# Optimization experiments

Measured on AMD Instinct MI355X. Metric: run time of the kernel, lower is better.

## Reference

```python
import jax, jax.numpy as jnp
import numpy as np

N_NODES = 50000
N_EDGES = 800000
D = 512
N_LAYERS = 3
LN_EPS = 1e-5


def _layer_norm(h, gamma, beta):
    mu = jnp.mean(h, axis=-1, keepdims=True)
    var = jnp.mean(jnp.square(h - mu), axis=-1, keepdims=True)
    return (h - mu) * jax.lax.rsqrt(var + LN_EPS) * gamma + beta


def setup_inputs() -> dict:
    key = jax.random.key(0)
    ks = jax.random.split(key, 5)
    x = jax.random.normal(ks[0], (N_NODES, D), dtype=jnp.float32)
    edge_index = jax.random.randint(ks[1], (2, N_EDGES), 0, N_NODES, dtype=jnp.int64)
    edge_weight = jax.random.uniform(ks[2], (N_EDGES,), dtype=jnp.float32)
    # GCNConv lin weights (xavier-ish scale), zero biases; LayerNorm affine params
    Ws = jax.random.normal(ks[3], (N_LAYERS, D, D), dtype=jnp.float32) * (1.0 / np.sqrt(D))
    bs = jnp.zeros((N_LAYERS, D), dtype=jnp.float32)
    gammas = jnp.ones((N_LAYERS, D), dtype=jnp.float32)
    betas = jnp.zeros((N_LAYERS, D), dtype=jnp.float32)
    return {"x": x, "edge_index": edge_index, "edge_weight": edge_weight,
            "Ws": Ws, "bs": bs, "gammas": gammas, "betas": betas}


def reference(x, edge_index, edge_weight, Ws, bs, gammas, betas):
    n = x.shape[0]
    row, col = edge_index[0], edge_index[1]  # source -> target (PyG convention)
    # add self loops with weight 1 (GCNConv add_self_loops=True)
    sl = jnp.arange(n, dtype=edge_index.dtype)
    row2 = jnp.concatenate([row, sl])
    col2 = jnp.concatenate([col, sl])
    ew = jnp.concatenate([edge_weight, jnp.ones((n,), dtype=edge_weight.dtype)])
    # symmetric normalization: D^{-1/2} A D^{-1/2}
    deg = jax.ops.segment_sum(ew, col2, num_segments=n)
    dinv = jnp.where(deg > 0, 1.0 / jnp.sqrt(jnp.where(deg > 0, deg, 1.0)), 0.0)
    norm = dinv[row2] * ew * dinv[col2]  # [E+N]

    for i in range(N_LAYERS):
        identity = x
        h = x @ Ws[i].T                       # [N, D] linear transform
        msg = norm[:, None] * h[row2]         # gather + scale per edge
        agg = jax.ops.segment_sum(msg, col2, num_segments=n) + bs[i]
        h = _layer_norm(agg, gammas[i], betas[i])
        if i < N_LAYERS - 1:
            h = jax.nn.relu(h)                # dropout=0 -> identity
        x = h + identity                      # residual (dims equal -> Identity proj)
    return x
```

## Files before the change

kernel.cpp:

```cpp
#include <hip/hip_runtime.h>
#include <hip/hip_bf16.h>
#include <stdint.h>

#define D 512
#define LN_EPS 1e-5f

typedef __attribute__((ext_vector_type(8))) short bf16x8;
typedef __attribute__((ext_vector_type(4))) float f32x4;

__device__ __forceinline__ unsigned short f32_to_bf16_bits(float x) {
    unsigned int u = __float_as_uint(x);
    u += 0x7fffu + ((u >> 16) & 1u);
    return (unsigned short)(u >> 16);
}
__device__ __forceinline__ float bf16lo(unsigned int u) { return __uint_as_float(u << 16); }
__device__ __forceinline__ float bf16hi(unsigned int u) { return __uint_as_float(u & 0xffff0000u); }

typedef const __attribute__((address_space(1))) unsigned int GU;
typedef __attribute__((address_space(3))) unsigned int LU;
__device__ __forceinline__ void gload_lds16(const void* g, void* l) {
    __builtin_amdgcn_global_load_lds((GU*)g, (LU*)l, 16, 0, 0);
}

__global__ void k_prep(const float4* __restrict__ x0, ushort4* __restrict__ xb4,
                       const float4* __restrict__ Ws4, ushort4* __restrict__ wb4,
                       float* __restrict__ deg, int* __restrict__ cnt,
                       long nx4, long nxin4, long nw4, int N) {
    long id = (long)blockIdx.x * blockDim.x + threadIdx.x;
    if (id < nx4) {
        float4 v;
        if (id < nxin4) v = x0[id];
        else { v.x = 0.f; v.y = 0.f; v.z = 0.f; v.w = 0.f; }
        ushort4 o;
        o.x = f32_to_bf16_bits(v.x);
        o.y = f32_to_bf16_bits(v.y);
        o.z = f32_to_bf16_bits(v.z);
        o.w = f32_to_bf16_bits(v.w);
        xb4[id] = o;
    } else if (id < nx4 + nw4) {
        long i = id - nx4;
        float4 v = Ws4[i];
        ushort4 o;
        o.x = f32_to_bf16_bits(v.x);
        o.y = f32_to_bf16_bits(v.y);
        o.z = f32_to_bf16_bits(v.z);
        o.w = f32_to_bf16_bits(v.w);
        wb4[i] = o;
    } else {
        long i = id - nx4 - nw4;
        if (i < N) { deg[i] = 1.0f; cnt[i] = 1; }
    }
}

__global__ void k_deg_cnt(const int* __restrict__ col, const float* __restrict__ ew,
                          float* deg, int* cnt, int E) {
    int e = blockIdx.x * blockDim.x + threadIdx.x;
    if (e < E) {
        int c = col[e];
        atomicAdd(&deg[c], ew[e]);
        atomicAdd(&cnt[c], 1);
    }
}

__global__ __launch_bounds__(1024) void k_scan(const int* __restrict__ cnt,
                                               float* __restrict__ deg,
                                               int* __restrict__ rptr,
                                               int* __restrict__ cur, int n) {
    for (int i = threadIdx.x; i < n; i += 1024) deg[i] = rsqrtf(deg[i]);

    const int tid = threadIdx.x, lane = tid & 63, wv = tid >> 6;
    const int chunk = (n + 15) >> 4;
    const int wbeg = wv * chunk;
    const int wend = min(wbeg + chunk, n);

    int tot = 0;
    for (int i = wbeg + lane; i < wend; i += 64) tot += cnt[i];
#pragma unroll
    for (int off = 32; off > 0; off >>= 1) tot += __shfl_xor(tot, off);
    __shared__ int woff[17];
    if (lane == 0) woff[wv] = tot;
    __syncthreads();
    if (tid == 0) {
        int r = 0;
        for (int w = 0; w < 16; ++w) { int t = woff[w]; woff[w] = r; r += t; }
        woff[16] = r;
    }
    __syncthreads();

    int run = woff[wv];
    for (int base = wbeg; base < wend; base += 64) {
        int i = base + lane;
        int v = (i < wend) ? cnt[i] : 0;
        int inc = v;
#pragma unroll
        for (int off = 1; off < 64; off <<= 1) {
            int u = __shfl_up(inc, off);
            if (lane >= off) inc += u;
        }
        if (i < wend) {
            int excl = run + inc - v;
            rptr[i] = excl;
            cur[i] = excl;
        }
        run += __shfl(inc, 63);
    }
    if (tid == 0) rptr[n] = woff[16];
}

__global__ void k_fill(const int* __restrict__ row, const int* __restrict__ col,
                       const float* __restrict__ ew, const float* __restrict__ dinv,
                       int* cur, uint2* __restrict__ srcval, int N, int E) {
    int i = blockIdx.x * blockDim.x + threadIdx.x;
    if (i < N) {
        int slot = atomicAdd(&cur[i], 1);
        float d = dinv[i];
        uint2 sv; sv.x = (unsigned)i; sv.y = __float_as_uint(d * d);
        srcval[slot] = sv;
    } else if (i < N + E) {
        int e = i - N;
        int r = row[e], c = col[e];
        int slot = atomicAdd(&cur[c], 1);
        uint2 sv; sv.x = (unsigned)r;
        sv.y = __float_as_uint(dinv[r] * ew[e] * dinv[c]);
        srcval[slot] = sv;
    }
}

__global__ __launch_bounds__(512) void k_gemm(
    const short* __restrict__ A,
    const short* __restrict__ W,
    short* __restrict__ H,
    int Mpad) {
    __shared__ short As[2][128 * 32];
    __shared__ short Bs[2][256 * 32];
    const int tid = threadIdx.x;
    const int wave = tid >> 6, lane = tid & 63;
    const int wm = (wave >> 2) * 64, wn = (wave & 3) * 64;
    const int tm = blockIdx.x * 128, tn = blockIdx.y * 256;
    f32x4 acc[4][4] = {};
    const int fr = lane & 15, fc = lane >> 4;

    const int r0 = tid >> 2, cb0 = (tid & 3) * 8;
    const short* Ab = A + (size_t)(tm + r0) * 512 + cb0;
    const short* Wb = W + (size_t)(tn + r0) * 512 + cb0;

    gload_lds16(Ab,                     &As[0][tid * 8]);
    gload_lds16(Wb,                     &Bs[0][tid * 8]);
    gload_lds16(Wb + (size_t)128 * 512, &Bs[0][(tid + 512) * 8]);
    __syncthreads();

    int cur = 0;
    for (int k0 = 0; k0 < 512; k0 += 32) {
        const int kn = k0 + 32;
        if (kn < 512) {
            gload_lds16(Ab + kn,                     &As[cur ^ 1][tid * 8]);
            gload_lds16(Wb + kn,                     &Bs[cur ^ 1][tid * 8]);
            gload_lds16(Wb + (size_t)128 * 512 + kn, &Bs[cur ^ 1][(tid + 512) * 8]);
        }
        bf16x8 af[4], bfr[4];
#pragma unroll
        for (int m = 0; m < 4; ++m)
            af[m] = *(const bf16x8*)&As[cur][(wm + m * 16 + fr) * 32 + fc * 8];
#pragma unroll
        for (int n = 0; n < 4; ++n)
            bfr[n] = *(const bf16x8*)&Bs[cur][(wn + n * 16 + fr) * 32 + fc * 8];
#pragma unroll
        for (int m = 0; m < 4; ++m) {
#pragma unroll
            for (int n = 0; n < 4; ++n)
                acc[m][n] = __builtin_amdgcn_mfma_f32_16x16x32_bf16(af[m], bfr[n], acc[m][n], 0, 0, 0);
        }
        __syncthreads();
        cur ^= 1;
    }
    const int cbase = tn + wn + (lane & 15);
    const int rbase = tm + wm + fc * 4;
#pragma unroll
    for (int m = 0; m < 4; ++m) {
#pragma unroll
        for (int n = 0; n < 4; ++n) {
#pragma unroll
            for (int j = 0; j < 4; ++j) {
                int r = rbase + m * 16 + j;
                int c = cbase + n * 16;
                H[(size_t)r * 512 + c] = (short)f32_to_bf16_bits(acc[m][n][j]);
            }
        }
    }
}

__global__ __launch_bounds__(256) void k_agg_ln(
    const uint4* __restrict__ H4,
    const int* __restrict__ rptr,
    const uint2* __restrict__ srcval,
    const float4* __restrict__ bias,
    const float4* __restrict__ gamma,
    const float4* __restrict__ beta,
    uint4* __restrict__ xb,
    float4* __restrict__ out_f32,
    int N, int last) {
    const int wv = threadIdx.x >> 6, lane = threadIdx.x & 63;
    const int t = blockIdx.x * 4 + wv;
    if (t >= N) return;
    const int beg = rptr[t], end = rptr[t + 1];

    float a[8], b[8];
#pragma unroll
    for (int i = 0; i < 8; ++i) { a[i] = 0.f; b[i] = 0.f; }

    for (int base = beg; base < end; base += 64) {
        int m = end - base;
        if (m > 64) m = 64;
        int idx = base + lane;
        if (idx > end - 1) idx = end - 1;
        uint2 svl = srcval[idx];
        int e = 0;
        for (; e + 2 <= m; e += 2) {
            unsigned s0 = __shfl(svl.x, e);
            unsigned s1 = __shfl(svl.x, e + 1);
            float w0 = __uint_as_float(__shfl(svl.y, e));
            float w1 = __uint_as_float(__shfl(svl.y, e + 1));
            uint4 u0 = H4[(size_t)s0 * 64 + lane];
            uint4 u1 = H4[(size_t)s1 * 64 + lane];
            a[0] = fmaf(w0, bf16lo(u0.x), a[0]);
            a[1] = fmaf(w0, bf16hi(u0.x), a[1]);
            a[2] = fmaf(w0, bf16lo(u0.y), a[2]);
            a[3] = fmaf(w0, bf16hi(u0.y), a[3]);
            a[4] = fmaf(w0, bf16lo(u0.z), a[4]);
            a[5] = fmaf(w0, bf16hi(u0.z), a[5]);
            a[6] = fmaf(w0, bf16lo(u0.w), a[6]);
            a[7] = fmaf(w0, bf16hi(u0.w), a[7]);
            b[0] = fmaf(w1, bf16lo(u1.x), b[0]);
            b[1] = fmaf(w1, bf16hi(u1.x), b[1]);
            b[2] = fmaf(w1, bf16lo(u1.y), b[2]);
            b[3] = fmaf(w1, bf16hi(u1.y), b[3]);
            b[4] = fmaf(w1, bf16lo(u1.z), b[4]);
            b[5] = fmaf(w1, bf16hi(u1.z), b[5]);
            b[6] = fmaf(w1, bf16lo(u1.w), b[6]);
            b[7] = fmaf(w1, bf16hi(u1.w), b[7]);
        }
        if (e < m) {
            unsigned s0 = __shfl(svl.x, e);
            float w0 = __uint_as_float(__shfl(svl.y, e));
            uint4 u0 = H4[(size_t)s0 * 64 + lane];
            a[0] = fmaf(w0, bf16lo(u0.x), a[0]);
            a[1] = fmaf(w0, bf16hi(u0.x), a[1]);
            a[2] = fmaf(w0, bf16lo(u0.y), a[2]);
            a[3] = fmaf(w0, bf16hi(u0.y), a[3]);
            a[4] = fmaf(w0, bf16lo(u0.z), a[4]);
            a[5] = fmaf(w0, bf16hi(u0.z), a[5]);
            a[6] = fmaf(w0, bf16lo(u0.w), a[6]);
            a[7] = fmaf(w0, bf16hi(u0.w), a[7]);
        }
    }
#pragma unroll
    for (int i = 0; i < 8; ++i) a[i] += b[i];

    float4 bv0 = bias[lane * 2], bv1 = bias[lane * 2 + 1];
    a[0] += bv0.x; a[1] += bv0.y; a[2] += bv0.z; a[3] += bv0.w;
    a[4] += bv1.x; a[5] += bv1.y; a[6] += bv1.z; a[7] += bv1.w;

    float s1 = 0.f, s2 = 0.f;
#pragma unroll
    for (int i = 0; i < 8; ++i) { s1 += a[i]; s2 += a[i] * a[i]; }
#pragma unroll
    for (int off = 32; off > 0; off >>= 1) {
        s1 += __shfl_xor(s1, off);
        s2 += __shfl_xor(s2, off);
    }
    const float mean = s1 * (1.0f / 512.0f);
    const float var = s2 * (1.0f / 512.0f) - mean * mean;
    const float rstd = rsqrtf(var + LN_EPS);

    float4 gv0 = gamma[lane * 2], gv1 = gamma[lane * 2 + 1];
    float4 bt0 = beta[lane * 2], bt1 = beta[lane * 2 + 1];
    float o[8];
    o[0] = (a[0] - mean) * rstd * gv0.x + bt0.x;
    o[1] = (a[1] - mean) * rstd * gv0.y + bt0.y;
    o[2] = (a[2] - mean) * rstd * gv0.z + bt0.z;
    o[3] = (a[3] - mean) * rstd * gv0.w + bt0.w;
    o[4] = (a[4] - mean) * rstd * gv1.x + bt1.x;
    o[5] = (a[5] - mean) * rstd * gv1.y + bt1.y;
    o[6] = (a[6] - mean) * rstd * gv1.z + bt1.z;
    o[7] = (a[7] - mean) * rstd * gv1.w + bt1.w;
    if (!last) {
#pragma unroll
        for (int i = 0; i < 8; ++i) o[i] = fmaxf(o[i], 0.f);
    }
    uint4 idu = xb[(size_t)t * 64 + lane];
    o[0] += bf16lo(idu.x); o[1] += bf16hi(idu.x);
    o[2] += bf16lo(idu.y); o[3] += bf16hi(idu.y);
    o[4] += bf16lo(idu.z); o[5] += bf16hi(idu.z);
    o[6] += bf16lo(idu.w); o[7] += bf16hi(idu.w);

    if (last) {
        float4 f0, f1;
        f0.x = o[0]; f0.y = o[1]; f0.z = o[2]; f0.w = o[3];
        f1.x = o[4]; f1.y = o[5]; f1.z = o[6]; f1.w = o[7];
        out_f32[(size_t)t * 128 + lane * 2] = f0;
        out_f32[(size_t)t * 128 + lane * 2 + 1] = f1;
    } else {
        uint4 pk;
        pk.x = ((unsigned)f32_to_bf16_bits(o[1]) << 16) | f32_to_bf16_bits(o[0]);
        pk.y = ((unsigned)f32_to_bf16_bits(o[3]) << 16) | f32_to_bf16_bits(o[2]);
        pk.z = ((unsigned)f32_to_bf16_bits(o[5]) << 16) | f32_to_bf16_bits(o[4]);
        pk.w = ((unsigned)f32_to_bf16_bits(o[7]) << 16) | f32_to_bf16_bits(o[6]);
        xb[(size_t)t * 64 + lane] = pk;
    }
}

extern "C" void kernel_launch(void* const* d_in, const int* in_sizes, int n_in,
                              void* d_out, int out_size, void* d_ws, size_t ws_size,
                              hipStream_t stream) {
    const float* x0     = (const float*)d_in[0];
    const int*   ei     = (const int*)d_in[1];
    const float* ew     = (const float*)d_in[2];
    const float* Ws     = (const float*)d_in[3];
    const float* bs     = (const float*)d_in[4];
    const float* gammas = (const float*)d_in[5];
    const float* betas  = (const float*)d_in[6];

    const int N = in_sizes[0] / D;
    const int E = in_sizes[1] / 2;
    const int L = in_sizes[3] / (D * D);
    const int Mpad = (N + 127) & ~127;

    char* p = (char*)d_ws;
    auto carve = [&](size_t bytes) {
        char* q = p;
        p += (bytes + 255) & ~(size_t)255;
        return (void*)q;
    };
    short* xb     = (short*)carve((size_t)Mpad * D * 2);
    short* hb     = (short*)carve((size_t)Mpad * D * 2);
    short* wb     = (short*)carve((size_t)L * D * D * 2);
    float* dinv   = (float*)carve((size_t)N * 4);
    int*   cnt    = (int*)carve((size_t)N * 4);
    int*   rptr   = (int*)carve((size_t)(N + 1) * 4);
    int*   cur    = (int*)carve((size_t)N * 4);
    uint2* srcval = (uint2*)carve((size_t)(E + N) * 8);
    (void)ws_size; (void)n_in; (void)out_size;

    const int* rowI = ei;
    const int* colI = ei + E;

    {
        long nx4 = (long)Mpad * D / 4, nxin4 = (long)N * D / 4;
        long nw4 = (long)L * D * D / 4;
        long tot = nx4 + nw4 + N;
        k_prep<<<(int)((tot + 255) / 256), 256, 0, stream>>>(
            (const float4*)x0, (ushort4*)xb, (const float4*)Ws, (ushort4*)wb,
            dinv, cnt, nx4, nxin4, nw4, N);
    }
    k_deg_cnt<<<(E + 255) / 256, 256, 0, stream>>>(colI, ew, dinv, cnt, E);
    k_scan<<<1, 1024, 0, stream>>>(cnt, dinv, rptr, cur, N);
    k_fill<<<(N + E + 255) / 256, 256, 0, stream>>>(rowI, colI, ew, dinv, cur, srcval, N, E);

    for (int l = 0; l < L; ++l) {
        dim3 g(Mpad / 128, D / 256);
        k_gemm<<<g, 512, 0, stream>>>(xb, wb + (size_t)l * D * D, hb, Mpad);
        int last = (l == L - 1);
        k_agg_ln<<<(N + 3) / 4, 256, 0, stream>>>(
            (const uint4*)hb, rptr, srcval,
            (const float4*)(bs + (size_t)l * D),
            (const float4*)(gammas + (size_t)l * D),
            (const float4*)(betas + (size_t)l * D),
            (uint4*)xb, (float4*)d_out, N, last);
    }
}
```

Measured before the change: 700.2 us.

## Aggregate before the linear transform and fuse LayerNorm into the GEMM epilogue

Uses linearity to compute the sparse aggregation on the bf16 node features first, then multiplies by W. Each GEMM block now covers all 512 output columns, so bias, LayerNorm (row stats reduced via LDS), ReLU and the residual run in the GEMM epilogue. This replaces the separate pass over the GEMM output. In exchange, each GEMM block holds twice the accumulators and LDS and there are half as many blocks, which risks load imbalance and lower occupancy. The epilogue also reads and writes xb as scattered 2-byte elements.

Result: slower. 893.3 us (+27.6%).

```diff
diff --git a/kernel.cpp b/kernel.cpp
--- a/kernel.cpp
+++ b/kernel.cpp
@@ -15,6 +15,7 @@
 }
 __device__ __forceinline__ float bf16lo(unsigned int u) { return __uint_as_float(u << 16); }
 __device__ __forceinline__ float bf16hi(unsigned int u) { return __uint_as_float(u & 0xffff0000u); }
+__device__ __forceinline__ float bf16s(short s) { return __uint_as_float(((unsigned int)(unsigned short)s) << 16); }
 
 typedef const __attribute__((address_space(1))) unsigned int GU;
 typedef __attribute__((address_space(3))) unsigned int LU;
@@ -126,79 +127,12 @@
     }
 }
 
-__global__ __launch_bounds__(512) void k_gemm(
-    const short* __restrict__ A,
-    const short* __restrict__ W,
-    short* __restrict__ H,
-    int Mpad) {
-    __shared__ short As[2][128 * 32];
-    __shared__ short Bs[2][256 * 32];
-    const int tid = threadIdx.x;
-    const int wave = tid >> 6, lane = tid & 63;
-    const int wm = (wave >> 2) * 64, wn = (wave & 3) * 64;
-    const int tm = blockIdx.x * 128, tn = blockIdx.y * 256;
-    f32x4 acc[4][4] = {};
-    const int fr = lane & 15, fc = lane >> 4;
-
-    const int r0 = tid >> 2, cb0 = (tid & 3) * 8;
-    const short* Ab = A + (size_t)(tm + r0) * 512 + cb0;
-    const short* Wb = W + (size_t)(tn + r0) * 512 + cb0;
-
-    gload_lds16(Ab,                     &As[0][tid * 8]);
-    gload_lds16(Wb,                     &Bs[0][tid * 8]);
-    gload_lds16(Wb + (size_t)128 * 512, &Bs[0][(tid + 512) * 8]);
-    __syncthreads();
-
-    int cur = 0;
-    for (int k0 = 0; k0 < 512; k0 += 32) {
-        const int kn = k0 + 32;
-        if (kn < 512) {
-            gload_lds16(Ab + kn,                     &As[cur ^ 1][tid * 8]);
-            gload_lds16(Wb + kn,                     &Bs[cur ^ 1][tid * 8]);
-            gload_lds16(Wb + (size_t)128 * 512 + kn, &Bs[cur ^ 1][(tid + 512) * 8]);
-        }
-        bf16x8 af[4], bfr[4];
-#pragma unroll
-        for (int m = 0; m < 4; ++m)
-            af[m] = *(const bf16x8*)&As[cur][(wm + m * 16 + fr) * 32 + fc * 8];
-#pragma unroll
-        for (int n = 0; n < 4; ++n)
-            bfr[n] = *(const bf16x8*)&Bs[cur][(wn + n * 16 + fr) * 32 + fc * 8];
-#pragma unroll
-        for (int m = 0; m < 4; ++m) {
-#pragma unroll
-            for (int n = 0; n < 4; ++n)
-                acc[m][n] = __builtin_amdgcn_mfma_f32_16x16x32_bf16(af[m], bfr[n], acc[m][n], 0, 0, 0);
-        }
-        __syncthreads();
-        cur ^= 1;
-    }
-    const int cbase = tn + wn + (lane & 15);
-    const int rbase = tm + wm + fc * 4;
-#pragma unroll
-    for (int m = 0; m < 4; ++m) {
-#pragma unroll
-        for (int n = 0; n < 4; ++n) {
-#pragma unroll
-            for (int j = 0; j < 4; ++j) {
-                int r = rbase + m * 16 + j;
-                int c = cbase + n * 16;
-                H[(size_t)r * 512 + c] = (short)f32_to_bf16_bits(acc[m][n][j]);
-            }
-        }
-    }
-}
-
-__global__ __launch_bounds__(256) void k_agg_ln(
-    const uint4* __restrict__ H4,
+__global__ __launch_bounds__(256) void k_agg(
+    const uint4* __restrict__ X4,
     const int* __restrict__ rptr,
     const uint2* __restrict__ srcval,
-    const float4* __restrict__ bias,
-    const float4* __restrict__ gamma,
-    const float4* __restrict__ beta,
-    uint4* __restrict__ xb,
-    float4* __restrict__ out_f32,
-    int N, int last) {
+    uint4* __restrict__ G4,
+    int N) {
     const int wv = threadIdx.x >> 6, lane = threadIdx.x & 63;
     const int t = blockIdx.x * 4 + wv;
     if (t >= N) return;
@@ -220,8 +154,8 @@
             unsigned s1 = __shfl(svl.x, e + 1);
             float w0 = __uint_as_float(__shfl(svl.y, e));
             float w1 = __uint_as_float(__shfl(svl.y, e + 1));
-            uint4 u0 = H4[(size_t)s0 * 64 + lane];
-            uint4 u1 = H4[(size_t)s1 * 64 + lane];
+            uint4 u0 = X4[(size_t)s0 * 64 + lane];
+            uint4 u1 = X4[(size_t)s1 * 64 + lane];
             a[0] = fmaf(w0, bf16lo(u0.x), a[0]);
             a[1] = fmaf(w0, bf16hi(u0.x), a[1]);
             a[2] = fmaf(w0, bf16lo(u0.y), a[2]);
@@ -242,7 +176,7 @@
         if (e < m) {
             unsigned s0 = __shfl(svl.x, e);
             float w0 = __uint_as_float(__shfl(svl.y, e));
-            uint4 u0 = H4[(size_t)s0 * 64 + lane];
+            uint4 u0 = X4[(size_t)s0 * 64 + lane];
             a[0] = fmaf(w0, bf16lo(u0.x), a[0]);
             a[1] = fmaf(w0, bf16hi(u0.x), a[1]);
             a[2] = fmaf(w0, bf16lo(u0.y), a[2]);
@@ -256,56 +190,142 @@
 #pragma unroll
     for (int i = 0; i < 8; ++i) a[i] += b[i];
 
-    float4 bv0 = bias[lane * 2], bv1 = bias[lane * 2 + 1];
-    a[0] += bv0.x; a[1] += bv0.y; a[2] += bv0.z; a[3] += bv0.w;
-    a[4] += bv1.x; a[5] += bv1.y; a[6] += bv1.z; a[7] += bv1.w;
-
-    float s1 = 0.f, s2 = 0.f;
-#pragma unroll
-    for (int i = 0; i < 8; ++i) { s1 += a[i]; s2 += a[i] * a[i]; }
-#pragma unroll
-    for (int off = 32; off > 0; off >>= 1) {
-        s1 += __shfl_xor(s1, off);
-        s2 += __shfl_xor(s2, off);
-    }
-    const float mean = s1 * (1.0f / 512.0f);
-    const float var = s2 * (1.0f / 512.0f) - mean * mean;
-    const float rstd = rsqrtf(var + LN_EPS);
-
-    float4 gv0 = gamma[lane * 2], gv1 = gamma[lane * 2 + 1];
-    float4 bt0 = beta[lane * 2], bt1 = beta[lane * 2 + 1];
-    float o[8];
-    o[0] = (a[0] - mean) * rstd * gv0.x + bt0.x;
-    o[1] = (a[1] - mean) * rstd * gv0.y + bt0.y;
-    o[2] = (a[2] - mean) * rstd * gv0.z + bt0.z;
-    o[3] = (a[3] - mean) * rstd * gv0.w + bt0.w;
-    o[4] = (a[4] - mean) * rstd * gv1.x + bt1.x;
-    o[5] = (a[5] - mean) * rstd * gv1.y + bt1.y;
-    o[6] = (a[6] - mean) * rstd * gv1.z + bt1.z;
-    o[7] = (a[7] - mean) * rstd * gv1.w + bt1.w;
-    if (!last) {
-#pragma unroll
-        for (int i = 0; i < 8; ++i) o[i] = fmaxf(o[i], 0.f);
-    }
-    uint4 idu = xb[(size_t)t * 64 + lane];
-    o[0] += bf16lo(idu.x); o[1] += bf16hi(idu.x);
-    o[2] += bf16lo(idu.y); o[3] += bf16hi(idu.y);
-    o[4] += bf16lo(idu.z); o[5] += bf16hi(idu.z);
-    o[6] += bf16lo(idu.w); o[7] += bf16hi(idu.w);
-
-    if (last) {
-        float4 f0, f1;
-        f0.x = o[0]; f0.y = o[1]; f0.z = o[2]; f0.w = o[3];
-        f1.x = o[4]; f1.y = o[5]; f1.z = o[6]; f1.w = o[7];
-        out_f32[(size_t)t * 128 + lane * 2] = f0;
-        out_f32[(size_t)t * 128 + lane * 2 + 1] = f1;
-    } else {
-        uint4 pk;
-        pk.x = ((unsigned)f32_to_bf16_bits(o[1]) << 16) | f32_to_bf16_bits(o[0]);
-        pk.y = ((unsigned)f32_to_bf16_bits(o[3]) << 16) | f32_to_bf16_bits(o[2]);
-        pk.z = ((unsigned)f32_to_bf16_bits(o[5]) << 16) | f32_to_bf16_bits(o[4]);
-        pk.w = ((unsigned)f32_to_bf16_bits(o[7]) << 16) | f32_to_bf16_bits(o[6]);
-        xb[(size_t)t * 64 + lane] = pk;
+    uint4 pk;
+    pk.x = ((unsigned)f32_to_bf16_bits(a[1]) << 16) | f32_to_bf16_bits(a[0]);
+    pk.y = ((unsigned)f32_to_bf16_bits(a[3]) << 16) | f32_to_bf16_bits(a[2]);
+    pk.z = ((unsigned)f32_to_bf16_bits(a[5]) << 16) | f32_to_bf16_bits(a[4]);
+    pk.w = ((unsigned)f32_to_bf16_bits(a[7]) << 16) | f32_to_bf16_bits(a[6]);
+    G4[(size_t)t * 64 + lane] = pk;
+}
+
+__global__ __launch_bounds__(512) void k_gemm_ln(
+    const short* __restrict__ A,
+    const short* __restrict__ W,
+    const float* __restrict__ bias,
+    const float* __restrict__ gamma,
+    const float* __restrict__ beta,
+    short* __restrict__ xb,
+    float* __restrict__ out_f32,
+    int N, int last) {
+    __shared__ short As[2][128 * 32];
+    __shared__ short Bs[2][512 * 32];
+    const int tid = threadIdx.x;
+    const int wave = tid >> 6, lane = tid & 63;
+    const int wmg = wave >> 2, wng = wave & 3;
+    const int wm = wmg * 64, wn0 = wng * 128;
+    const int tm = blockIdx.x * 128;
+    f32x4 acc[4][8] = {};
+    const int fr = lane & 15, fc = lane >> 4;
+
+    const int r0 = tid >> 2, cb0 = (tid & 3) * 8;
+    const short* Ab = A + (size_t)(tm + r0) * 512 + cb0;
+    const short* Wb = W + (size_t)r0 * 512 + cb0;
+
+    gload_lds16(Ab,                     &As[0][tid * 8]);
+    gload_lds16(Wb,                     &Bs[0][tid * 8]);
+    gload_lds16(Wb + (size_t)128 * 512, &Bs[0][(tid + 512) * 8]);
+    gload_lds16(Wb + (size_t)256 * 512, &Bs[0][(tid + 1024) * 8]);
+    gload_lds16(Wb + (size_t)384 * 512, &Bs[0][(tid + 1536) * 8]);
+    __syncthreads();
+
+    int cur = 0;
+    for (int k0 = 0; k0 < 512; k0 += 32) {
+        const int kn = k0 + 32;
+        if (kn < 512) {
+            gload_lds16(Ab + kn,                     &As[cur ^ 1][tid * 8]);
+            gload_lds16(Wb + kn,                     &Bs[cur ^ 1][tid * 8]);
+            gload_lds16(Wb + (size_t)128 * 512 + kn, &Bs[cur ^ 1][(tid + 512) * 8]);
+            gload_lds16(Wb + (size_t)256 * 512 + kn, &Bs[cur ^ 1][(tid + 1024) * 8]);
+            gload_lds16(Wb + (size_t)384 * 512 + kn, &Bs[cur ^ 1][(tid + 1536) * 8]);
+        }
+        bf16x8 af[4], bfr[8];
+#pragma unroll
+        for (int m = 0; m < 4; ++m)
+            af[m] = *(const bf16x8*)&As[cur][(wm + m * 16 + fr) * 32 + fc * 8];
+#pragma unroll
+        for (int n = 0; n < 8; ++n)
+            bfr[n] = *(const bf16x8*)&Bs[cur][(wn0 + n * 16 + fr) * 32 + fc * 8];
+#pragma unroll
+        for (int m = 0; m < 4; ++m) {
+#pragma unroll
+            for (int n = 0; n < 8; ++n)
+                acc[m][n] = __builtin_amdgcn_mfma_f32_16x16x32_bf16(af[m], bfr[n], acc[m][n], 0, 0, 0);
+        }
+        __syncthreads();
+        cur ^= 1;
+    }
+
+    float2* part  = (float2*)&As[0][0];
+    float2* stats = (float2*)&As[1][0];
+
+    const int c0 = wn0 + fr;
+    float bv[8], gv[8], btv[8];
+#pragma unroll
+    for (int n = 0; n < 8; ++n) {
+        bv[n]  = bias[c0 + n * 16];
+        gv[n]  = gamma[c0 + n * 16];
+        btv[n] = beta[c0 + n * 16];
+    }
+#pragma unroll
+    for (int m = 0; m < 4; ++m) {
+#pragma unroll
+        for (int j = 0; j < 4; ++j) {
+            float s1 = 0.f, s2 = 0.f;
+#pragma unroll
+            for (int n = 0; n < 8; ++n) {
+                float v = acc[m][n][j] + bv[n];
+                s1 += v;
+                s2 += v * v;
+            }
+#pragma unroll
+            for (int off = 1; off < 16; off <<= 1) {
+                s1 += __shfl_xor(s1, off);
+                s2 += __shfl_xor(s2, off);
+            }
+            if (fr == 0) {
+                float2 p; p.x = s1; p.y = s2;
+                part[(wmg * 4 + wng) * 64 + fc * 4 + m * 16 + j] = p;
+            }
+        }
+    }
+    __syncthreads();
+    if (tid < 128) {
+        int rl = tid & 63, g = tid >> 6;
+        float s1 = 0.f, s2 = 0.f;
+#pragma unroll
+        for (int w = 0; w < 4; ++w) {
+            float2 p = part[(g * 4 + w) * 64 + rl];
+            s1 += p.x; s2 += p.y;
+        }
+        float mean = s1 * (1.0f / 512.0f);
+        float var = s2 * (1.0f / 512.0f) - mean * mean;
+        float2 st; st.x = mean; st.y = rsqrtf(var + LN_EPS);
+        stats[g * 64 + rl] = st;
+    }
+    __syncthreads();
+
+#pragma unroll
+    for (int m = 0; m < 4; ++m) {
+#pragma unroll
+        for (int j = 0; j < 4; ++j) {
+            const int rl = fc * 4 + m * 16 + j;
+            const float2 st = stats[wmg * 64 + rl];
+            const int r = tm + wm + rl;
+            const size_t rb = (size_t)r * 512;
+#pragma unroll
+            for (int n = 0; n < 8; ++n) {
+                const int c = c0 + n * 16;
+                float v = acc[m][n][j] + bv[n];
+                float o = (v - st.x) * st.y * gv[n] + btv[n];
+                if (!last) o = fmaxf(o, 0.f);
+                o += bf16s(xb[rb + c]);
+                if (last) {
+                    if (r < N) out_f32[rb + c] = o;
+                } else {
+                    xb[rb + c] = (short)f32_to_bf16_bits(o);
+                }
+            }
+        }
     }
 }
 
@@ -332,7 +352,7 @@
         return (void*)q;
     };
     short* xb     = (short*)carve((size_t)Mpad * D * 2);
-    short* hb     = (short*)carve((size_t)Mpad * D * 2);
+    short* gb     = (short*)carve((size_t)Mpad * D * 2);
     short* wb     = (short*)carve((size_t)L * D * D * 2);
     float* dinv   = (float*)carve((size_t)N * 4);
     int*   cnt    = (int*)carve((size_t)N * 4);
@@ -357,14 +377,12 @@
     k_fill<<<(N + E + 255) / 256, 256, 0, stream>>>(rowI, colI, ew, dinv, cur, srcval, N, E);
 
     for (int l = 0; l < L; ++l) {
-        dim3 g(Mpad / 128, D / 256);
-        k_gemm<<<g, 512, 0, stream>>>(xb, wb + (size_t)l * D * D, hb, Mpad);
         int last = (l == L - 1);
-        k_agg_ln<<<(N + 3) / 4, 256, 0, stream>>>(
-            (const uint4*)hb, rptr, srcval,
-            (const float4*)(bs + (size_t)l * D),
-            (const float4*)(gammas + (size_t)l * D),
-            (const float4*)(betas + (size_t)l * D),
-            (uint4*)xb, (float4*)d_out, N, last);
-    }
-}
+        k_agg<<<(N + 3) / 4, 256, 0, stream>>>(
+            (const uint4*)xb, rptr, srcval, (uint4*)gb, N);
+        k_gemm_ln<<<Mpad / 128, 512, 0, stream>>>(
+            gb, wb + (size_t)l * D * D,
+            bs + (size_t)l * D, gammas + (size_t)l * D, betas + (size_t)l * D,
+            xb, (float*)d_out, N, last);
+    }
+}
```

## Triple-buffer GEMM LDS pipeline and move degree rsqrt out of single-block scan

Applied to the files above, without the earlier changes.

The GEMM moves from double to triple LDS buffering. It uses explicit vmcnt waits and a single barrier per k-step, so global loads run two stages ahead and the trailing syncthreads goes away. Separately, the rsqrt over all node degrees leaves the single-block scan kernel and is recomputed per edge inside k_fill, which shortens the serial one-block kernel at the cost of two rsqrts per edge. LDS use grows to 72KB per block, which may limit occupancy.

New measurement: 685.2 us. 2.1% less time.

```diff
diff --git a/kernel.cpp b/kernel.cpp
--- a/kernel.cpp
+++ b/kernel.cpp
@@ -63,11 +63,8 @@
 }
 
 __global__ __launch_bounds__(1024) void k_scan(const int* __restrict__ cnt,
-                                               float* __restrict__ deg,
                                                int* __restrict__ rptr,
                                                int* __restrict__ cur, int n) {
-    for (int i = threadIdx.x; i < n; i += 1024) deg[i] = rsqrtf(deg[i]);
-
     const int tid = threadIdx.x, lane = tid & 63, wv = tid >> 6;
     const int chunk = (n + 15) >> 4;
     const int wbeg = wv * chunk;
@@ -108,20 +105,19 @@
 }
 
 __global__ void k_fill(const int* __restrict__ row, const int* __restrict__ col,
-                       const float* __restrict__ ew, const float* __restrict__ dinv,
+                       const float* __restrict__ ew, const float* __restrict__ deg,
                        int* cur, uint2* __restrict__ srcval, int N, int E) {
     int i = blockIdx.x * blockDim.x + threadIdx.x;
     if (i < N) {
         int slot = atomicAdd(&cur[i], 1);
-        float d = dinv[i];
-        uint2 sv; sv.x = (unsigned)i; sv.y = __float_as_uint(d * d);
+        uint2 sv; sv.x = (unsigned)i; sv.y = __float_as_uint(1.0f / deg[i]);
         srcval[slot] = sv;
     } else if (i < N + E) {
         int e = i - N;
         int r = row[e], c = col[e];
         int slot = atomicAdd(&cur[c], 1);
         uint2 sv; sv.x = (unsigned)r;
-        sv.y = __float_as_uint(dinv[r] * ew[e] * dinv[c]);
+        sv.y = __float_as_uint(rsqrtf(deg[r]) * ew[e] * rsqrtf(deg[c]));
         srcval[slot] = sv;
     }
 }
@@ -131,8 +127,8 @@
     const short* __restrict__ W,
     short* __restrict__ H,
     int Mpad) {
-    __shared__ short As[2][128 * 32];
-    __shared__ short Bs[2][256 * 32];
+    __shared__ short As[3][128 * 32];
+    __shared__ short Bs[3][256 * 32];
     const int tid = threadIdx.x;
     const int wave = tid >> 6, lane = tid & 63;
     const int wm = (wave >> 2) * 64, wn = (wave & 3) * 64;
@@ -144,35 +140,39 @@
     const short* Ab = A + (size_t)(tm + r0) * 512 + cb0;
     const short* Wb = W + (size_t)(tn + r0) * 512 + cb0;
 
-    gload_lds16(Ab,                     &As[0][tid * 8]);
-    gload_lds16(Wb,                     &Bs[0][tid * 8]);
-    gload_lds16(Wb + (size_t)128 * 512, &Bs[0][(tid + 512) * 8]);
-    __syncthreads();
-
-    int cur = 0;
-    for (int k0 = 0; k0 < 512; k0 += 32) {
-        const int kn = k0 + 32;
-        if (kn < 512) {
-            gload_lds16(Ab + kn,                     &As[cur ^ 1][tid * 8]);
-            gload_lds16(Wb + kn,                     &Bs[cur ^ 1][tid * 8]);
-            gload_lds16(Wb + (size_t)128 * 512 + kn, &Bs[cur ^ 1][(tid + 512) * 8]);
-        }
+#define STAGE(t)                                                            \
+    {                                                                       \
+        const int _k = (t) * 32, _b = (t) % 3;                              \
+        gload_lds16(Ab + _k,                     &As[_b][tid * 8]);         \
+        gload_lds16(Wb + _k,                     &Bs[_b][tid * 8]);         \
+        gload_lds16(Wb + (size_t)128 * 512 + _k, &Bs[_b][(tid + 512) * 8]); \
+    }
+
+    STAGE(0);
+    STAGE(1);
+#pragma unroll
+    for (int t = 0; t < 16; ++t) {
+        if (t < 15) asm volatile("s_waitcnt vmcnt(3)" ::: "memory");
+        else        asm volatile("s_waitcnt vmcnt(0)" ::: "memory");
+        __builtin_amdgcn_s_barrier();
+        asm volatile("" ::: "memory");
+        if (t < 14) STAGE(t + 2);
+        const int b = t % 3;
         bf16x8 af[4], bfr[4];
 #pragma unroll
         for (int m = 0; m < 4; ++m)
-            af[m] = *(const bf16x8*)&As[cur][(wm + m * 16 + fr) * 32 + fc * 8];
+            af[m] = *(const bf16x8*)&As[b][(wm + m * 16 + fr) * 32 + fc * 8];
 #pragma unroll
         for (int n = 0; n < 4; ++n)
-            bfr[n] = *(const bf16x8*)&Bs[cur][(wn + n * 16 + fr) * 32 + fc * 8];
+            bfr[n] = *(const bf16x8*)&Bs[b][(wn + n * 16 + fr) * 32 + fc * 8];
 #pragma unroll
         for (int m = 0; m < 4; ++m) {
 #pragma unroll
             for (int n = 0; n < 4; ++n)
                 acc[m][n] = __builtin_amdgcn_mfma_f32_16x16x32_bf16(af[m], bfr[n], acc[m][n], 0, 0, 0);
         }
-        __syncthreads();
-        cur ^= 1;
-    }
+    }
+#undef STAGE
     const int cbase = tn + wn + (lane & 15);
     const int rbase = tm + wm + fc * 4;
 #pragma unroll
@@ -334,7 +334,7 @@
     short* xb     = (short*)carve((size_t)Mpad * D * 2);
     short* hb     = (short*)carve((size_t)Mpad * D * 2);
     short* wb     = (short*)carve((size_t)L * D * D * 2);
-    float* dinv   = (float*)carve((size_t)N * 4);
+    float* deg    = (float*)carve((size_t)N * 4);
     int*   cnt    = (int*)carve((size_t)N * 4);
     int*   rptr   = (int*)carve((size_t)(N + 1) * 4);
     int*   cur    = (int*)carve((size_t)N * 4);
@@ -350,11 +350,11 @@
         long tot = nx4 + nw4 + N;
         k_prep<<<(int)((tot + 255) / 256), 256, 0, stream>>>(
             (const float4*)x0, (ushort4*)xb, (const float4*)Ws, (ushort4*)wb,
-            dinv, cnt, nx4, nxin4, nw4, N);
-    }
-    k_deg_cnt<<<(E + 255) / 256, 256, 0, stream>>>(colI, ew, dinv, cnt, E);
-    k_scan<<<1, 1024, 0, stream>>>(cnt, dinv, rptr, cur, N);
-    k_fill<<<(N + E + 255) / 256, 256, 0, stream>>>(rowI, colI, ew, dinv, cur, srcval, N, E);
+            deg, cnt, nx4, nxin4, nw4, N);
+    }
+    k_deg_cnt<<<(E + 255) / 256, 256, 0, stream>>>(colI, ew, deg, cnt, E);
+    k_scan<<<1, 1024, 0, stream>>>(cnt, rptr, cur, N);
+    k_fill<<<(N + E + 255) / 256, 256, 0, stream>>>(rowI, colI, ew, deg, cur, srcval, N, E);
 
     for (int l = 0; l < L; ++l) {
         dim3 g(Mpad / 128, D / 256);
```
